# Kernel optimization log

Hardware: AMD Instinct MI355X
Metric: run time of the kernel (lower is better)

Reference implementation:

```python
import jax, jax.numpy as jnp
import numpy as np

WS = 7  # window size

def _relative_position_index(ws):
    ch, cw = np.arange(ws), np.arange(ws)
    coords = np.stack(np.meshgrid(ch, cw, indexing='ij'))  # (2, ws, ws)
    cf = coords.reshape(2, -1)                              # (2, N)
    rel = cf[:, :, None] - cf[:, None, :]                   # (2, N, N)
    rel = rel.transpose(1, 2, 0).astype(np.int32)           # (N, N, 2)
    rel[:, :, 0] += ws - 1
    rel[:, :, 1] += ws - 1
    rel[:, :, 0] *= 2 * ws - 1
    return rel.sum(-1)                                      # (N, N)

def setup_inputs() -> dict:
    key = jax.random.key(0)
    ks = jax.random.split(key, 5)
    B_, N, C, nW = 4096, WS * WS, 192, 64
    x = jax.random.normal(ks[0], (B_, N, C), dtype=jnp.float32)
    mask = jnp.zeros((nW, N, N), dtype=jnp.float32)
    rel_bias_table = jax.random.normal(ks[1], ((2 * WS - 1) ** 2, 6), jnp.float32) * 0.02
    qkv_w = jax.random.normal(ks[2], (3 * C, C), jnp.float32) * 0.05
    qkv_b = jnp.zeros((3 * C,), jnp.float32)
    proj_w = jax.random.normal(ks[3], (C, C), jnp.float32) * 0.05
    proj_b = jnp.zeros((C,), jnp.float32)
    rel_index = jnp.asarray(_relative_position_index(WS))
    return {"x": x, "mask": mask, "rel_bias_table": rel_bias_table,
            "qkv_w": qkv_w, "qkv_b": qkv_b, "proj_w": proj_w,
            "proj_b": proj_b, "rel_index": rel_index, "window_size": WS}

def reference(x, mask, rel_bias_table, qkv_w, qkv_b, proj_w, proj_b, rel_index, window_size):
    B_, N, C = x.shape
    n_head = rel_bias_table.shape[1]
    hd = C // n_head
    scale = hd ** (-0.5)
    qkv = x @ qkv_w.T + qkv_b                                # (B_, N, 3C)
    qkv = qkv.reshape(B_, N, 3, n_head, hd).transpose(2, 0, 3, 1, 4)
    q, k, v = qkv[0] * scale, qkv[1], qkv[2]                 # (B_, h, N, hd)
    attn = jnp.einsum('bhnd,bhmd->bhnm', q, k)               # (B_, h, N, N)
    bias = rel_bias_table[rel_index.reshape(-1)].reshape(N, N, n_head)
    attn = attn + bias.transpose(2, 0, 1)[None]              # add rel-pos bias
    nW = mask.shape[0]
    attn = attn.reshape(B_ // nW, nW, n_head, N, N) + mask[None, :, None]
    attn = jax.nn.softmax(attn.reshape(B_, n_head, N, N), axis=-1)
    out = jnp.einsum('bhnm,bhmd->bhnd', attn, v)             # (B_, h, N, hd)
    out = out.transpose(0, 2, 1, 3).reshape(B_, N, C)
    out = out @ proj_w.T + proj_b
    return out
```

## Files before the change

kernel.cpp:

```cpp
#include <hip/hip_runtime.h>
#include <hip/hip_bf16.h>

#define TN 49
#define TC 192
#define NH 6
#define HD 32
#define NP 64
#define XSTR 200
#define QSTR 40
#define VSTR 72
#define PSTR 72
#define WSTR 200

typedef __bf16 bf16x8 __attribute__((ext_vector_type(8)));
typedef float  f32x4  __attribute__((ext_vector_type(4)));

static constexpr float SCALE = 0.17677669529663687f;

__device__ __forceinline__ unsigned short f2bf(float f) {
    union { float f; unsigned u; } v; v.f = f;
    unsigned r = v.u + 0x7FFFu + ((v.u >> 16) & 1u);
    return (unsigned short)(r >> 16);
}

__global__ __launch_bounds__(256) void wconv_kernel(
    const float* __restrict__ qw, const float* __restrict__ pw,
    unsigned short* __restrict__ qwb, unsigned short* __restrict__ pwb)
{
    int idx = blockIdx.x * 256 + threadIdx.x;
    if (idx < 576 * 192) qwb[idx] = f2bf(qw[idx]);
    else {
        int j = idx - 576 * 192;
        if (j < 192 * 192) pwb[j] = f2bf(pw[j]);
    }
}

__global__ __launch_bounds__(256) void attn_kernel(
    const float* __restrict__ x, const float* __restrict__ mask,
    const float* __restrict__ bt, const unsigned short* __restrict__ wqkv,
    const float* __restrict__ qb, const int* __restrict__ ridx,
    unsigned short* __restrict__ ao, int nW)
{
    __shared__ __align__(16) unsigned short Xs[NP * XSTR];
    __shared__ __align__(16) unsigned short Qh[NP * QSTR];
    __shared__ __align__(16) unsigned short Kh[NP * QSTR];
    __shared__ __align__(16) unsigned short VT[HD * VSTR];
    __shared__ __align__(16) unsigned short PW[32 * WSTR];

    unsigned short* Wsh = PW;
    unsigned short* Ps  = PW;

    const int b    = blockIdx.x;
    const int t    = threadIdx.x;
    const int w    = t >> 6;
    const int lane = t & 63;
    const int l15  = lane & 15;
    const int quad = lane >> 4;
    const float NEG_INF = -__builtin_inff();

    {
        const float4* xg = (const float4*)(x + (size_t)b * TN * TC);
        for (int idx = t; idx < NP * (TC / 4); idx += 256) {
            int row = idx / (TC / 4), c4 = idx % (TC / 4);
            unsigned o0 = 0, o1 = 0;
            if (row < TN) {
                float4 v = xg[row * (TC / 4) + c4];
                o0 = (unsigned)f2bf(v.x) | ((unsigned)f2bf(v.y) << 16);
                o1 = (unsigned)f2bf(v.z) | ((unsigned)f2bf(v.w) << 16);
            }
            uint2 u; u.x = o0; u.y = o1;
            *(uint2*)&Xs[row * XSTR + c4 * 4] = u;
        }
    }
    __syncthreads();

    bf16x8 af[6];
#pragma unroll
    for (int kt = 0; kt < 6; ++kt)
        af[kt] = *(const bf16x8*)&Xs[(w * 16 + l15) * XSTR + kt * 32 + quad * 8];

    const float* maskp = mask + (size_t)(b % nW) * TN * TN;

#pragma unroll 1
    for (int h = 0; h < NH; ++h) {
#pragma unroll 1
        for (int mat = 0; mat < 3; ++mat) {
            __syncthreads();
            const uint4* wg = (const uint4*)(wqkv + (size_t)(mat * TC + h * HD) * TC);
            for (int idx = t; idx < 32 * 24; idx += 256) {
                int row = idx / 24, c8 = idx % 24;
                *(uint4*)&Wsh[row * WSTR + c8 * 8] = wg[idx];
            }
            __syncthreads();
#pragma unroll
            for (int ct = 0; ct < 2; ++ct) {
                f32x4 acc = {0.f, 0.f, 0.f, 0.f};
#pragma unroll
                for (int kt = 0; kt < 6; ++kt) {
                    bf16x8 bf = *(const bf16x8*)&Wsh[(ct * 16 + l15) * WSTR + kt * 32 + quad * 8];
                    acc = __builtin_amdgcn_mfma_f32_16x16x32_bf16(af[kt], bf, acc, 0, 0, 0);
                }
                const int d = ct * 16 + l15;
                const float bias = qb[mat * TC + h * HD + d];
#pragma unroll
                for (int r = 0; r < 4; ++r) {
                    int n = w * 16 + quad * 4 + r;
                    float val = acc[r] + bias;
                    if (mat == 0)      Qh[n * QSTR + d] = f2bf(val * SCALE);
                    else if (mat == 1) Kh[n * QSTR + d] = f2bf(val);
                    else               VT[d * VSTR + n] = f2bf(val);
                }
            }
        }
        __syncthreads();

        bf16x8 aq = *(const bf16x8*)&Qh[(w * 16 + l15) * QSTR + quad * 8];
        f32x4 sacc[4];
#pragma unroll
        for (int tc = 0; tc < 4; ++tc) {
            bf16x8 bk = *(const bf16x8*)&Kh[(tc * 16 + l15) * QSTR + quad * 8];
            f32x4 z = {0.f, 0.f, 0.f, 0.f};
            sacc[tc] = __builtin_amdgcn_mfma_f32_16x16x32_bf16(aq, bk, z, 0, 0, 0);
        }

        float sv[4][4];
        float mx[4] = {NEG_INF, NEG_INF, NEG_INF, NEG_INF};
#pragma unroll
        for (int tc = 0; tc < 4; ++tc) {
            int m = tc * 16 + l15;
#pragma unroll
            for (int r = 0; r < 4; ++r) {
                int n = w * 16 + quad * 4 + r;
                float s;
                if (m < TN) {
                    s = sacc[tc][r];
                    if (n < TN) {
                        int flat = n * TN + m;
                        s += bt[ridx[flat] * NH + h] + maskp[flat];
                    }
                } else s = NEG_INF;
                sv[tc][r] = s;
                mx[r] = fmaxf(mx[r], s);
            }
        }
#pragma unroll
        for (int r = 0; r < 4; ++r) {
            mx[r] = fmaxf(mx[r], __shfl_xor(mx[r], 1));
            mx[r] = fmaxf(mx[r], __shfl_xor(mx[r], 2));
            mx[r] = fmaxf(mx[r], __shfl_xor(mx[r], 4));
            mx[r] = fmaxf(mx[r], __shfl_xor(mx[r], 8));
        }
        float sm[4] = {0.f, 0.f, 0.f, 0.f};
#pragma unroll
        for (int tc = 0; tc < 4; ++tc)
#pragma unroll
            for (int r = 0; r < 4; ++r) {
                float p = __expf(sv[tc][r] - mx[r]);
                sv[tc][r] = p;
                sm[r] += p;
            }
#pragma unroll
        for (int r = 0; r < 4; ++r) {
            sm[r] += __shfl_xor(sm[r], 1);
            sm[r] += __shfl_xor(sm[r], 2);
            sm[r] += __shfl_xor(sm[r], 4);
            sm[r] += __shfl_xor(sm[r], 8);
            sm[r] = 1.0f / sm[r];
        }
#pragma unroll
        for (int tc = 0; tc < 4; ++tc)
#pragma unroll
            for (int r = 0; r < 4; ++r)
                Ps[(w * 16 + quad * 4 + r) * PSTR + tc * 16 + l15] = f2bf(sv[tc][r] * sm[r]);

#pragma unroll
        for (int dt = 0; dt < 2; ++dt) {
            f32x4 pacc = {0.f, 0.f, 0.f, 0.f};
#pragma unroll
            for (int kt = 0; kt < 2; ++kt) {
                bf16x8 ap = *(const bf16x8*)&Ps[(w * 16 + l15) * PSTR + kt * 32 + quad * 8];
                bf16x8 bv = *(const bf16x8*)&VT[(dt * 16 + l15) * VSTR + kt * 32 + quad * 8];
                pacc = __builtin_amdgcn_mfma_f32_16x16x32_bf16(ap, bv, pacc, 0, 0, 0);
            }
#pragma unroll
            for (int r = 0; r < 4; ++r) {
                int n = w * 16 + quad * 4 + r;
                if (n < TN) {
                    int c = h * HD + dt * 16 + l15;
                    ao[((size_t)b * TN + n) * TC + c] = f2bf(pacc[r]);
                }
            }
        }
    }
}

__global__ __launch_bounds__(256) void proj_kernel(
    const unsigned short* __restrict__ ao, const unsigned short* __restrict__ wp,
    const float* __restrict__ pb, float* __restrict__ out, int M)
{
    __shared__ __align__(16) unsigned short As[NP * XSTR];

    const int blk  = blockIdx.x;
    const int t    = threadIdx.x;
    const int w    = t >> 6;
    const int lane = t & 63;
    const int l15  = lane & 15;
    const int quad = lane >> 4;

    {
        const uint4* ag = (const uint4*)(ao + (size_t)blk * 64 * TC);
        for (int idx = t; idx < 64 * 24; idx += 256) {
            int row = idx / 24, c8 = idx % 24;
            uint4 v = {0, 0, 0, 0};
            if (blk * 64 + row < M) v = ag[idx];
            *(uint4*)&As[row * XSTR + c8 * 8] = v;
        }
    }
    __syncthreads();

    bf16x8 af[6];
#pragma unroll
    for (int kt = 0; kt < 6; ++kt)
        af[kt] = *(const bf16x8*)&As[(w * 16 + l15) * XSTR + kt * 32 + quad * 8];

#pragma unroll 1
    for (int ct = 0; ct < 12; ++ct) {
        f32x4 acc = {0.f, 0.f, 0.f, 0.f};
#pragma unroll
        for (int kt = 0; kt < 6; ++kt) {
            bf16x8 bf = *(const bf16x8*)(wp + (size_t)(ct * 16 + l15) * TC + kt * 32 + quad * 8);
            acc = __builtin_amdgcn_mfma_f32_16x16x32_bf16(af[kt], bf, acc, 0, 0, 0);
        }
        const int c = ct * 16 + l15;
        const float bias = pb[c];
#pragma unroll
        for (int r = 0; r < 4; ++r) {
            int gm = blk * 64 + w * 16 + quad * 4 + r;
            if (gm < M) out[(size_t)gm * TC + c] = acc[r] + bias;
        }
    }
}

extern "C" void kernel_launch(void* const* d_in, const int* in_sizes, int n_in,
                              void* d_out, int out_size, void* d_ws, size_t ws_size,
                              hipStream_t stream) {
    const float* x    = (const float*)d_in[0];
    const float* mask = (const float*)d_in[1];
    const float* bt   = (const float*)d_in[2];
    const float* qw   = (const float*)d_in[3];
    const float* qb   = (const float*)d_in[4];
    const float* pw   = (const float*)d_in[5];
    const float* pb   = (const float*)d_in[6];
    const int*   ridx = (const int*)d_in[7];

    const int B  = in_sizes[0] / (TN * TC);
    const int nW = in_sizes[1] / (TN * TN);
    const int M  = B * TN;

    unsigned short* wqkvb = (unsigned short*)d_ws;
    unsigned short* wpb   = wqkvb + 576 * 192;
    unsigned short* ao    = wpb + 192 * 192;

    hipLaunchKernelGGL(wconv_kernel, dim3(576), dim3(256), 0, stream,
                       qw, pw, wqkvb, wpb);
    hipLaunchKernelGGL(attn_kernel, dim3(B), dim3(256), 0, stream,
                       x, mask, bt, wqkvb, qb, ridx, ao, nW);
    hipLaunchKernelGGL(proj_kernel, dim3((M + 63) / 64), dim3(256), 0, stream,
                       ao, wpb, pb, (float*)d_out, M);
}
```

Measured before the change: 757.0 us.

## Fuse projection into attention kernel and precompute combined bias-mask table

Merges the attention and output-projection kernels into one per-window kernel, so the bf16 attention output no longer round-trips through global memory. All QKV heads are computed up front, with weights read directly from global memory instead of being staged through shared memory per head. This removes the many per-head barriers of the old design. A small pre-kernel builds a combined relative-bias plus mask table, replacing the per-element index gathers inside the softmax. Shared memory use grows to roughly 79KB per block, with launch bounds requesting two blocks per CU, which may limit occupancy.

```diff
diff --git a/kernel.cpp b/kernel.cpp
--- a/kernel.cpp
+++ b/kernel.cpp
@@ -4,13 +4,10 @@
 #define TN 49
 #define TC 192
 #define NH 6
-#define HD 32
 #define NP 64
-#define XSTR 200
-#define QSTR 40
+#define NN (TN*TN)
+#define SSTR 200
 #define VSTR 72
-#define PSTR 72
-#define WSTR 200
 
 typedef __bf16 bf16x8 __attribute__((ext_vector_type(8)));
 typedef float  f32x4  __attribute__((ext_vector_type(4)));
@@ -35,20 +32,28 @@
     }
 }
 
-__global__ __launch_bounds__(256) void attn_kernel(
-    const float* __restrict__ x, const float* __restrict__ mask,
-    const float* __restrict__ bt, const unsigned short* __restrict__ wqkv,
-    const float* __restrict__ qb, const int* __restrict__ ridx,
-    unsigned short* __restrict__ ao, int nW)
+__global__ __launch_bounds__(256) void bias_kernel(
+    const float* __restrict__ bt, const int* __restrict__ ridx,
+    const float* __restrict__ mask, float* __restrict__ cmb, int total)
 {
-    __shared__ __align__(16) unsigned short Xs[NP * XSTR];
-    __shared__ __align__(16) unsigned short Qh[NP * QSTR];
-    __shared__ __align__(16) unsigned short Kh[NP * QSTR];
-    __shared__ __align__(16) unsigned short VT[HD * VSTR];
-    __shared__ __align__(16) unsigned short PW[32 * WSTR];
-
-    unsigned short* Wsh = PW;
-    unsigned short* Ps  = PW;
+    int idx = blockIdx.x * 256 + threadIdx.x;
+    if (idx >= total) return;
+    int nm = idx % NN;
+    int hw = idx / NN;
+    int h  = hw % NH;
+    int wi = hw / NH;
+    cmb[idx] = bt[ridx[nm] * NH + h] + mask[(size_t)wi * NN + nm];
+}
+
+__global__ __launch_bounds__(256, 2) void fused_kernel(
+    const float* __restrict__ x, const float* __restrict__ cmb,
+    const unsigned short* __restrict__ wqkv, const float* __restrict__ qb,
+    const unsigned short* __restrict__ wp, const float* __restrict__ pb,
+    float* __restrict__ out, int nW)
+{
+    __shared__ __align__(16) unsigned short SC[NP * SSTR];
+    __shared__ __align__(16) unsigned short KS[NP * SSTR];
+    __shared__ __align__(16) unsigned short VT[TC * VSTR];
 
     const int b    = blockIdx.x;
     const int t    = threadIdx.x;
@@ -56,6 +61,8 @@
     const int lane = t & 63;
     const int l15  = lane & 15;
     const int quad = lane >> 4;
+    const int row0 = w * 16 + quad * 4;
+    const int arow = w * 16 + l15;
     const float NEG_INF = -__builtin_inff();
 
     {
@@ -69,7 +76,7 @@
                 o1 = (unsigned)f2bf(v.z) | ((unsigned)f2bf(v.w) << 16);
             }
             uint2 u; u.x = o0; u.y = o1;
-            *(uint2*)&Xs[row * XSTR + c4 * 4] = u;
+            *(uint2*)&SC[row * SSTR + c4 * 4] = u;
         }
     }
     __syncthreads();
@@ -77,52 +84,71 @@
     bf16x8 af[6];
 #pragma unroll
     for (int kt = 0; kt < 6; ++kt)
-        af[kt] = *(const bf16x8*)&Xs[(w * 16 + l15) * XSTR + kt * 32 + quad * 8];
-
-    const float* maskp = mask + (size_t)(b % nW) * TN * TN;
-
-#pragma unroll 1
+        af[kt] = *(const bf16x8*)&SC[arow * SSTR + kt * 32 + quad * 8];
+
+#pragma unroll 3
+    for (int ct = 0; ct < 12; ++ct) {
+        f32x4 acc = {0.f, 0.f, 0.f, 0.f};
+        const unsigned short* wr = wqkv + (size_t)(ct * 16 + l15) * TC + quad * 8;
+#pragma unroll
+        for (int kt = 0; kt < 6; ++kt)
+            acc = __builtin_amdgcn_mfma_f32_16x16x32_bf16(
+                af[kt], *(const bf16x8*)(wr + kt * 32), acc, 0, 0, 0);
+        const int d = ct * 16 + l15;
+        const float bias = qb[d];
+#pragma unroll
+        for (int r = 0; r < 4; ++r)
+            SC[(row0 + r) * SSTR + d] = f2bf((acc[r] + bias) * SCALE);
+    }
+#pragma unroll 3
+    for (int ct = 0; ct < 12; ++ct) {
+        f32x4 acc = {0.f, 0.f, 0.f, 0.f};
+        const unsigned short* wr = wqkv + (size_t)(TC + ct * 16 + l15) * TC + quad * 8;
+#pragma unroll
+        for (int kt = 0; kt < 6; ++kt)
+            acc = __builtin_amdgcn_mfma_f32_16x16x32_bf16(
+                af[kt], *(const bf16x8*)(wr + kt * 32), acc, 0, 0, 0);
+        const int d = ct * 16 + l15;
+        const float bias = qb[TC + d];
+#pragma unroll
+        for (int r = 0; r < 4; ++r)
+            KS[(row0 + r) * SSTR + d] = f2bf(acc[r] + bias);
+    }
+#pragma unroll 3
+    for (int ct = 0; ct < 12; ++ct) {
+        f32x4 acc = {0.f, 0.f, 0.f, 0.f};
+        const unsigned short* wr = wqkv + (size_t)(2 * TC + ct * 16 + l15) * TC + quad * 8;
+#pragma unroll
+        for (int kt = 0; kt < 6; ++kt)
+            acc = __builtin_amdgcn_mfma_f32_16x16x32_bf16(
+                af[kt], *(const bf16x8*)(wr + kt * 32), acc, 0, 0, 0);
+        const int d = ct * 16 + l15;
+        const float bias = qb[2 * TC + d];
+#pragma unroll
+        for (int r = 0; r < 4; ++r)
+            VT[d * VSTR + row0 + r] = f2bf(acc[r] + bias);
+    }
+
+    bf16x8 aq[NH];
+#pragma unroll
+    for (int h = 0; h < NH; ++h)
+        aq[h] = *(const bf16x8*)&SC[arow * SSTR + h * 32 + quad * 8];
+
+    __syncthreads();
+
+    const float* cmbb = cmb + (size_t)((b % nW) * NH) * NN;
+    f32x4 oacc[NH][2];
+
+#pragma unroll
     for (int h = 0; h < NH; ++h) {
-#pragma unroll 1
-        for (int mat = 0; mat < 3; ++mat) {
-            __syncthreads();
-            const uint4* wg = (const uint4*)(wqkv + (size_t)(mat * TC + h * HD) * TC);
-            for (int idx = t; idx < 32 * 24; idx += 256) {
-                int row = idx / 24, c8 = idx % 24;
-                *(uint4*)&Wsh[row * WSTR + c8 * 8] = wg[idx];
-            }
-            __syncthreads();
-#pragma unroll
-            for (int ct = 0; ct < 2; ++ct) {
-                f32x4 acc = {0.f, 0.f, 0.f, 0.f};
-#pragma unroll
-                for (int kt = 0; kt < 6; ++kt) {
-                    bf16x8 bf = *(const bf16x8*)&Wsh[(ct * 16 + l15) * WSTR + kt * 32 + quad * 8];
-                    acc = __builtin_amdgcn_mfma_f32_16x16x32_bf16(af[kt], bf, acc, 0, 0, 0);
-                }
-                const int d = ct * 16 + l15;
-                const float bias = qb[mat * TC + h * HD + d];
-#pragma unroll
-                for (int r = 0; r < 4; ++r) {
-                    int n = w * 16 + quad * 4 + r;
-                    float val = acc[r] + bias;
-                    if (mat == 0)      Qh[n * QSTR + d] = f2bf(val * SCALE);
-                    else if (mat == 1) Kh[n * QSTR + d] = f2bf(val);
-                    else               VT[d * VSTR + n] = f2bf(val);
-                }
-            }
-        }
-        __syncthreads();
-
-        bf16x8 aq = *(const bf16x8*)&Qh[(w * 16 + l15) * QSTR + quad * 8];
         f32x4 sacc[4];
 #pragma unroll
         for (int tc = 0; tc < 4; ++tc) {
-            bf16x8 bk = *(const bf16x8*)&Kh[(tc * 16 + l15) * QSTR + quad * 8];
+            bf16x8 bk = *(const bf16x8*)&KS[(tc * 16 + l15) * SSTR + h * 32 + quad * 8];
             f32x4 z = {0.f, 0.f, 0.f, 0.f};
-            sacc[tc] = __builtin_amdgcn_mfma_f32_16x16x32_bf16(aq, bk, z, 0, 0, 0);
-        }
-
+            sacc[tc] = __builtin_amdgcn_mfma_f32_16x16x32_bf16(aq[h], bk, z, 0, 0, 0);
+        }
+        const float* cp = cmbb + (size_t)h * NN;
         float sv[4][4];
         float mx[4] = {NEG_INF, NEG_INF, NEG_INF, NEG_INF};
 #pragma unroll
@@ -130,15 +156,12 @@
             int m = tc * 16 + l15;
 #pragma unroll
             for (int r = 0; r < 4; ++r) {
-                int n = w * 16 + quad * 4 + r;
-                float s;
+                int n = row0 + r;
+                float s = NEG_INF;
                 if (m < TN) {
                     s = sacc[tc][r];
-                    if (n < TN) {
-                        int flat = n * TN + m;
-                        s += bt[ridx[flat] * NH + h] + maskp[flat];
-                    }
-                } else s = NEG_INF;
+                    if (n < TN) s += cp[n * TN + m];
+                }
                 sv[tc][r] = s;
                 mx[r] = fmaxf(mx[r], s);
             }
@@ -171,72 +194,49 @@
         for (int tc = 0; tc < 4; ++tc)
 #pragma unroll
             for (int r = 0; r < 4; ++r)
-                Ps[(w * 16 + quad * 4 + r) * PSTR + tc * 16 + l15] = f2bf(sv[tc][r] * sm[r]);
+                SC[(row0 + r) * SSTR + tc * 16 + l15] = f2bf(sv[tc][r] * sm[r]);
 
 #pragma unroll
         for (int dt = 0; dt < 2; ++dt) {
             f32x4 pacc = {0.f, 0.f, 0.f, 0.f};
 #pragma unroll
             for (int kt = 0; kt < 2; ++kt) {
-                bf16x8 ap = *(const bf16x8*)&Ps[(w * 16 + l15) * PSTR + kt * 32 + quad * 8];
-                bf16x8 bv = *(const bf16x8*)&VT[(dt * 16 + l15) * VSTR + kt * 32 + quad * 8];
+                bf16x8 ap = *(const bf16x8*)&SC[arow * SSTR + kt * 32 + quad * 8];
+                bf16x8 bv = *(const bf16x8*)&VT[(h * 32 + dt * 16 + l15) * VSTR + kt * 32 + quad * 8];
                 pacc = __builtin_amdgcn_mfma_f32_16x16x32_bf16(ap, bv, pacc, 0, 0, 0);
             }
-#pragma unroll
-            for (int r = 0; r < 4; ++r) {
-                int n = w * 16 + quad * 4 + r;
-                if (n < TN) {
-                    int c = h * HD + dt * 16 + l15;
-                    ao[((size_t)b * TN + n) * TC + c] = f2bf(pacc[r]);
-                }
-            }
-        }
-    }
-}
-
-__global__ __launch_bounds__(256) void proj_kernel(
-    const unsigned short* __restrict__ ao, const unsigned short* __restrict__ wp,
-    const float* __restrict__ pb, float* __restrict__ out, int M)
-{
-    __shared__ __align__(16) unsigned short As[NP * XSTR];
-
-    const int blk  = blockIdx.x;
-    const int t    = threadIdx.x;
-    const int w    = t >> 6;
-    const int lane = t & 63;
-    const int l15  = lane & 15;
-    const int quad = lane >> 4;
-
-    {
-        const uint4* ag = (const uint4*)(ao + (size_t)blk * 64 * TC);
-        for (int idx = t; idx < 64 * 24; idx += 256) {
-            int row = idx / 24, c8 = idx % 24;
-            uint4 v = {0, 0, 0, 0};
-            if (blk * 64 + row < M) v = ag[idx];
-            *(uint4*)&As[row * XSTR + c8 * 8] = v;
-        }
-    }
-    __syncthreads();
-
-    bf16x8 af[6];
+            oacc[h][dt] = pacc;
+        }
+    }
+
+#pragma unroll
+    for (int h = 0; h < NH; ++h)
+#pragma unroll
+        for (int dt = 0; dt < 2; ++dt)
+#pragma unroll
+            for (int r = 0; r < 4; ++r)
+                SC[(row0 + r) * SSTR + h * 32 + dt * 16 + l15] = f2bf(oacc[h][dt][r]);
+
+    bf16x8 pf[6];
 #pragma unroll
     for (int kt = 0; kt < 6; ++kt)
-        af[kt] = *(const bf16x8*)&As[(w * 16 + l15) * XSTR + kt * 32 + quad * 8];
-
-#pragma unroll 1
-    for (int ct = 0; ct < 12; ++ct) {
-        f32x4 acc = {0.f, 0.f, 0.f, 0.f};
-#pragma unroll
-        for (int kt = 0; kt < 6; ++kt) {
-            bf16x8 bf = *(const bf16x8*)(wp + (size_t)(ct * 16 + l15) * TC + kt * 32 + quad * 8);
-            acc = __builtin_amdgcn_mfma_f32_16x16x32_bf16(af[kt], bf, acc, 0, 0, 0);
-        }
+        pf[kt] = *(const bf16x8*)&SC[arow * SSTR + kt * 32 + quad * 8];
+
+#pragma unroll 3
+    for (int ct = 0; ct < 12; ++ct) {
+        f32x4 acc = {0.f, 0.f, 0.f, 0.f};
+        const unsigned short* wr = wp + (size_t)(ct * 16 + l15) * TC + quad * 8;
+#pragma unroll
+        for (int kt = 0; kt < 6; ++kt)
+            acc = __builtin_amdgcn_mfma_f32_16x16x32_bf16(
+                pf[kt], *(const bf16x8*)(wr + kt * 32), acc, 0, 0, 0);
         const int c = ct * 16 + l15;
         const float bias = pb[c];
 #pragma unroll
         for (int r = 0; r < 4; ++r) {
-            int gm = blk * 64 + w * 16 + quad * 4 + r;
-            if (gm < M) out[(size_t)gm * TC + c] = acc[r] + bias;
+            int n = row0 + r;
+            if (n < TN)
+                out[((size_t)b * TN + n) * TC + c] = acc[r] + bias;
         }
     }
 }
@@ -255,16 +255,17 @@
 
     const int B  = in_sizes[0] / (TN * TC);
     const int nW = in_sizes[1] / (TN * TN);
-    const int M  = B * TN;
 
     unsigned short* wqkvb = (unsigned short*)d_ws;
     unsigned short* wpb   = wqkvb + 576 * 192;
-    unsigned short* ao    = wpb + 192 * 192;
+    float*          cmb   = (float*)(wpb + 192 * 192);
+
+    const int total = nW * NH * NN;
 
     hipLaunchKernelGGL(wconv_kernel, dim3(576), dim3(256), 0, stream,
                        qw, pw, wqkvb, wpb);
-    hipLaunchKernelGGL(attn_kernel, dim3(B), dim3(256), 0, stream,
-                       x, mask, bt, wqkvb, qb, ridx, ao, nW);
-    hipLaunchKernelGGL(proj_kernel, dim3((M + 63) / 64), dim3(256), 0, stream,
-                       ao, wpb, pb, (float*)d_out, M);
-}
+    hipLaunchKernelGGL(bias_kernel, dim3((total + 255) / 256), dim3(256), 0, stream,
+                       bt, ridx, mask, cmb, total);
+    hipLaunchKernelGGL(fused_kernel, dim3(B), dim3(256), 0, stream,
+                       x, cmb, wqkvb, qb, wpb, pb, (float*)d_out, nW);
+}
```

Result: slower. 944.8 us (+24.8%).
